# Kernel tuning notes

Measured on AMD Instinct MI355X. Metric: run time of the kernel, lower is better.

Reference implementation:

```python
import jax, jax.numpy as jnp
import numpy as np

D_MODEL = 2048
NUM_HEADS = 16
HEAD_DIM = D_MODEL // NUM_HEADS


def setup_inputs() -> dict:
    key = jax.random.key(0)
    ks = jax.random.split(key, 11)
    B, S = 2, 2048
    s = 1.0 / np.sqrt(D_MODEL)
    return {
        "query": jax.random.normal(ks[0], (B, S, D_MODEL), jnp.float32),
        "key_in": jax.random.normal(ks[1], (B, S, D_MODEL), jnp.float32),
        "value": jax.random.normal(ks[2], (B, S, D_MODEL), jnp.float32),
        "Wq": jax.random.normal(ks[3], (D_MODEL, D_MODEL), jnp.float32) * s,
        "bq": jnp.zeros((D_MODEL,), jnp.float32),
        "Wk": jax.random.normal(ks[4], (D_MODEL, D_MODEL), jnp.float32) * s,
        "bk": jnp.zeros((D_MODEL,), jnp.float32),
        "Wv": jax.random.normal(ks[5], (D_MODEL, D_MODEL), jnp.float32) * s,
        "bv": jnp.zeros((D_MODEL,), jnp.float32),
        "Wo": jax.random.normal(ks[6], (D_MODEL, D_MODEL), jnp.float32) * s,
        "bo": jnp.zeros((D_MODEL,), jnp.float32),
    }


def reference(query, key_in, value, Wq, bq, Wk, bk, Wv, bv, Wo, bo):
    B, S, _ = query.shape
    # projections (torch Linear: x @ W.T + b)
    q = query @ Wq.T + bq
    k = key_in @ Wk.T + bk
    v = value @ Wv.T + bv
    # [B, H, S, Dh]
    q = q.reshape(B, S, NUM_HEADS, HEAD_DIM).transpose(0, 2, 1, 3)
    k = k.reshape(B, -1, NUM_HEADS, HEAD_DIM).transpose(0, 2, 1, 3)
    v = v.reshape(B, -1, NUM_HEADS, HEAD_DIM).transpose(0, 2, 1, 3)
    scores = jnp.einsum("bhqd,bhkd->bhqk", q, k) / np.sqrt(HEAD_DIM).astype(np.float32)
    attn = jax.nn.softmax(scores, axis=-1)
    out = jnp.einsum("bhqk,bhkd->bhqd", attn, v)
    out = out.transpose(0, 2, 1, 3).reshape(B, S, D_MODEL)
    return out @ Wo.T + bo
```

## Files before the change

### kernel.cpp

```cpp
#include <hip/hip_runtime.h>
#include <hip/hip_bf16.h>
#include <stdint.h>

typedef __hip_bfloat16 bf16;
typedef __attribute__((ext_vector_type(8))) short bf16x8;
typedef __attribute__((ext_vector_type(4))) float f32x4;
typedef __attribute__((ext_vector_type(4))) short s16x4;

constexpr int D_MODEL   = 2048;
constexpr int NUM_HEADS = 16;
constexpr int HEAD_DIM  = 128;
constexpr int BATCH     = 2;
constexpr int SEQ       = 2048;

constexpr int GBM = 256, GBN = 128, GBK = 64;
constexpr int G_ABUF = GBM * GBK;
constexpr int G_BBUF = GBN * GBK;
constexpr int G_BUF  = G_ABUF + G_BBUF;
constexpr int G_LDS  = 3 * G_BUF;

__device__ __forceinline__ void gload_lds16(const bf16* g, bf16* l) {
    __builtin_amdgcn_global_load_lds(
        (const __attribute__((address_space(1))) void*)g,
        (__attribute__((address_space(3))) void*)l, 16, 0, 0);
}

typedef __attribute__((address_space(3))) const bf16 lds_cbf16;

struct CvtArgs { const float* src[7]; bf16* dst[7]; int n8[7]; };

__global__ __launch_bounds__(256)
void cvt_multi(CvtArgs a)
{
    const int t = blockIdx.y;
    const float* __restrict__ s = a.src[t];
    bf16* __restrict__ d = a.dst[t];
    const int n8 = a.n8[t];
    for (int i = blockIdx.x * 256 + threadIdx.x; i < n8; i += gridDim.x * 256) {
        f32x4 x = *(const f32x4*)(s + (size_t)i * 8);
        f32x4 y = *(const f32x4*)(s + (size_t)i * 8 + 4);
        bf16 t8[8] = { __float2bfloat16(x[0]), __float2bfloat16(x[1]),
                       __float2bfloat16(x[2]), __float2bfloat16(x[3]),
                       __float2bfloat16(y[0]), __float2bfloat16(y[1]),
                       __float2bfloat16(y[2]), __float2bfloat16(y[3]) };
        *(bf16x8*)(d + (size_t)i * 8) = *(const bf16x8*)t8;
    }
}


#define DS_READ16(A0, B0, A1, B1, vA0, vB0, vA1, vB1)                          \
    asm volatile(                                                              \
        "ds_read_b128 %0, %16 offset:0\n\t"                                    \
        "ds_read_b128 %1, %16 offset:2048\n\t"                                 \
        "ds_read_b128 %2, %16 offset:4096\n\t"                                 \
        "ds_read_b128 %3, %16 offset:6144\n\t"                                 \
        "ds_read_b128 %4, %17 offset:0\n\t"                                    \
        "ds_read_b128 %5, %17 offset:2048\n\t"                                 \
        "ds_read_b128 %6, %17 offset:4096\n\t"                                 \
        "ds_read_b128 %7, %17 offset:6144\n\t"                                 \
        "ds_read_b128 %8, %18 offset:0\n\t"                                    \
        "ds_read_b128 %9, %18 offset:2048\n\t"                                 \
        "ds_read_b128 %10, %18 offset:4096\n\t"                                \
        "ds_read_b128 %11, %18 offset:6144\n\t"                                \
        "ds_read_b128 %12, %19 offset:0\n\t"                                   \
        "ds_read_b128 %13, %19 offset:2048\n\t"                                \
        "ds_read_b128 %14, %19 offset:4096\n\t"                                \
        "ds_read_b128 %15, %19 offset:6144"                                    \
        : "=&v"(A0[0]), "=&v"(A0[1]), "=&v"(A0[2]), "=&v"(A0[3]),              \
          "=&v"(B0[0]), "=&v"(B0[1]), "=&v"(B0[2]), "=&v"(B0[3]),              \
          "=&v"(A1[0]), "=&v"(A1[1]), "=&v"(A1[2]), "=&v"(A1[3]),              \
          "=&v"(B1[0]), "=&v"(B1[1]), "=&v"(B1[2]), "=&v"(B1[3])               \
        : "v"(vA0), "v"(vB0), "v"(vA1), "v"(vB1))

#define MFMA_HALF(AR, BR)                                                      \
    {                                                                          \
        __builtin_amdgcn_s_setprio(1);                                         \
        _Pragma("unroll")                                                      \
        for (int i_ = 0; i_ < 4; i_++)                                         \
            _Pragma("unroll")                                                  \
            for (int j_ = 0; j_ < 4; j_++)                                     \
                acc[i_][j_] = __builtin_amdgcn_mfma_f32_16x16x32_bf16(         \
                    AR[i_], BR[j_], acc[i_][j_], 0, 0, 0);                     \
        __builtin_amdgcn_s_setprio(0);                                         \
        __builtin_amdgcn_sched_barrier(0);                                     \
    }

#define GEMM_TILE(t, CA0, CB0, CA1, CB1, NA0, NB0, NA1, NB1)                   \
    {                                                                          \
        const int  bs_ = (bc + 2 >= 3) ? bc - 1 : bc + 2;                      \
        const bool pf_ = (t) + 2 < NT;                                         \
        if (pf_) { stageA((t) + 2, bs_, 0); stageA((t) + 2, bs_, 1);           \
                   stageA((t) + 2, bs_, 2); stageA((t) + 2, bs_, 3);           \
                   stageB((t) + 2, bs_, 0); stageB((t) + 2, bs_, 1); }         \
        asm volatile("s_waitcnt lgkmcnt(0)" ::: "memory");    \
        __builtin_amdgcn_sched_barrier(0);                                     \
        MFMA_HALF(CA0, CB0);                                                   \
        if (pf_)               asm volatile("s_waitcnt vmcnt(6)" ::: "memory");\
        else if ((t) + 1 < NT) asm volatile("s_waitcnt vmcnt(0)" ::: "memory");\
        asm volatile("s_barrier" ::: "memory");          \
        if ((t) + 1 < NT) {                                                    \
            const int bn_ = (bc + 1 >= 3) ? 0 : bc + 1;                        \
            const uint32_t nA_ = aoffTh + (uint32_t)(bn_ * (G_BUF * 2));       \
            const uint32_t nB_ = boffTh + (uint32_t)(bn_ * (G_BUF * 2));       \
            DS_READ16(NA0, NB0, NA1, NB1, nA_, nB_, nA_ ^ 64u, nB_ ^ 64u);     \
            __builtin_amdgcn_sched_barrier(0);        \
        }                                                                      \
        MFMA_HALF(CA1, CB1);                                                   \
        bc = (bc + 1 == 3) ? 0 : bc + 1;                                       \
    }

template <typename TC, bool TRANS_PERM>
__device__ __forceinline__
void gemm_body(const bf16* __restrict__ A, const bf16* __restrict__ W,
               const float* __restrict__ bias, TC* __restrict__ C,
               int M, int N, int K, bf16* smem)
{
    const int tid  = threadIdx.x;
    const int lane = tid & 63;
    const int wave = tid >> 6;
    const int quad = lane >> 4, l16 = lane & 15;
    const int sw   = l16 & 7;
    const int wr   = wave >> 1;
    const int wc   = wave & 1;
    const int m0   = blockIdx.y * GBM, n0 = blockIdx.x * GBN;

    const int rloc = tid >> 3;
    const int gsw  = (tid & 7) ^ (rloc & 7);
    const int NT   = K / GBK;

    const bf16* Abase = A + (size_t)(m0 + rloc) * K + gsw * 8;
    const bf16* Bbase = W + (size_t)(n0 + rloc) * K + gsw * 8;
    const size_t rstep = (size_t)64 * K;

    auto stageA = [&](int t, int bi, int u) {
        gload_lds16(Abase + u * rstep + (size_t)t * GBK,
                    smem + bi * G_BUF + (u * 512 + tid) * 8);
    };
    auto stageB = [&](int t, int bi, int u) {
        gload_lds16(Bbase + u * rstep + (size_t)t * GBK,
                    smem + bi * G_BUF + G_ABUF + (u * 512 + tid) * 8);
    };

    const uint32_t aoffTh = (uint32_t)(uintptr_t)(lds_cbf16*)
        &smem[(wr * 64 + l16) * 64 + (quad ^ sw) * 8];
    const uint32_t boffTh = (uint32_t)(uintptr_t)(lds_cbf16*)
        &smem[G_ABUF + (wc * 64 + l16) * 64 + (quad ^ sw) * 8];

    f32x4 acc[4][4];
#pragma unroll
    for (int i = 0; i < 4; i++)
#pragma unroll
        for (int j = 0; j < 4; j++) acc[i][j] = (f32x4){0.f, 0.f, 0.f, 0.f};

    bf16x8 pa0[4], pb0[4], pa1[4], pb1[4];
    bf16x8 qa0[4], qb0[4], qa1[4], qb1[4];

#pragma unroll
    for (int u = 0; u < 4; u++) stageA(0, 0, u);
#pragma unroll
    for (int u = 0; u < 2; u++) stageB(0, 0, u);
    if (NT > 1) {
#pragma unroll
        for (int u = 0; u < 4; u++) stageA(1, 1, u);
#pragma unroll
        for (int u = 0; u < 2; u++) stageB(1, 1, u);
        asm volatile("s_waitcnt vmcnt(6)" ::: "memory");
    } else {
        asm volatile("s_waitcnt vmcnt(0)" ::: "memory");
    }
    asm volatile("s_barrier" ::: "memory");
    DS_READ16(pa0, pb0, pa1, pb1, aoffTh, boffTh, aoffTh ^ 64u, boffTh ^ 64u);
    __builtin_amdgcn_sched_barrier(0);

    int bc = 0;
    for (int t = 0; t < NT; t += 2) {
        GEMM_TILE(t,     pa0, pb0, pa1, pb1,  qa0, qb0, qa1, qb1);
        GEMM_TILE(t + 1, qa0, qb0, qa1, qb1,  pa0, pb0, pa1, pb1);
    }

#pragma unroll
    for (int j = 0; j < 4; j++) {
        const int col = n0 + wc * 64 + j * 16 + l16;
        const float bv = bias[col];
#pragma unroll
        for (int i = 0; i < 4; i++) {
            const int row0 = m0 + wr * 64 + i * 16 + quad * 4;
            if constexpr (TRANS_PERM) {
                int g   = row0 & 63;
                int tau = g >> 4, qh = (g >> 2) & 3;
                int pp  = (tau >> 1) * 32 + qh * 8 + (tau & 1) * 4;
                int sp  = ((row0 & 2047) & ~63) | pp;
                size_t idx = (size_t)(row0 >> 11) * ((size_t)D_MODEL * SEQ)
                           + (size_t)col * SEQ + sp;
                bf16 t4[4];
#pragma unroll
                for (int r = 0; r < 4; r++) t4[r] = __float2bfloat16(acc[i][j][r] + bv);
                *(s16x4*)&C[idx] = *(const s16x4*)t4;
            } else {
#pragma unroll
                for (int r = 0; r < 4; r++) {
                    int row = row0 + r;
                    if constexpr (sizeof(TC) == 2)
                        C[(size_t)row * N + col] = (TC)__float2bfloat16(acc[i][j][r] + bv);
                    else
                        C[(size_t)row * N + col] = (TC)(acc[i][j][r] + bv);
                }
            }
        }
    }
}

template <typename TC, bool TRANS_PERM>
__global__ __launch_bounds__(512, 2)
void gemm_bf16(const bf16* __restrict__ A, const bf16* __restrict__ W,
               const float* __restrict__ bias, TC* __restrict__ C,
               int M, int N, int K)
{
    __shared__ bf16 smem[G_LDS];
    gemm_body<TC, TRANS_PERM>(A, W, bias, C, M, N, K, smem);
}

struct QkvArgs { const bf16* A[3]; const bf16* W[3]; const float* bias[3]; bf16* C[3]; };

__global__ __launch_bounds__(512, 2)
void gemm_qkv(QkvArgs ga, int M, int N, int K)
{
    __shared__ bf16 smem[G_LDS];
    const int z = blockIdx.z;
    if (z == 2) gemm_body<bf16, true >(ga.A[2], ga.W[2], ga.bias[2], ga.C[2], M, N, K, smem);
    else        gemm_body<bf16, false>(ga.A[z], ga.W[z], ga.bias[z], ga.C[z], M, N, K, smem);
}

struct QkArgs { const bf16* A[2]; const bf16* W[2]; const float* bias[2]; bf16* C[2]; };

__global__ __launch_bounds__(512, 2)
void gemm_qk(QkArgs ga, int M, int N, int K)
{
    __shared__ bf16 smem[G_LDS];
    const int z = blockIdx.z;
    gemm_body<bf16, false>(ga.A[z], ga.W[z], ga.bias[z], ga.C[z], M, N, K, smem);
}

__global__ __launch_bounds__(256)
void flash_attn_kernel(const bf16* __restrict__ Qp, const bf16* __restrict__ Kp,
                       const bf16* __restrict__ Vt, bf16* __restrict__ Op)
{
    constexpr int BQ = 128, BKV = 64, DH = 128;
    __shared__ bf16 sK[2][BKV * DH];
    __shared__ bf16 sV[2][DH * BKV];

    const int tid  = threadIdx.x;
    const int wave = tid >> 6, lane = tid & 63;
    const int quad = lane >> 4, l16 = lane & 15;
    const int q0 = blockIdx.x * BQ;
    const int h  = blockIdx.y;
    const int b  = blockIdx.z;

    const size_t base  = (size_t)b * SEQ * D_MODEL + (size_t)h * HEAD_DIM;
    const size_t basev = ((size_t)b * NUM_HEADS + h) * (size_t)HEAD_DIM * SEQ;
    const bf16* Kb = Kp + base;
    const bf16* Vb = Vt + basev;

    auto stage = [&](int t, int bi) {
        const bf16* Kt = Kb + (size_t)t * BKV * D_MODEL;
        const bf16* Vtile = Vb + (size_t)t * BKV;
        bf16* sKb = sK[bi];
        bf16* sVb = sV[bi];
#pragma unroll
        for (int s = 0; s < 4; s++) {
            int c = s * 256 + wave * 64 + lane;
            int row = c >> 4, gs = c & 15;
            int g = gs ^ (row & 15);
            gload_lds16(Kt + (size_t)row * D_MODEL + g * 8, sKb + (size_t)c * 8);
        }
#pragma unroll
        for (int s = 0; s < 4; s++) {
            int c = s * 256 + wave * 64 + lane;
            int dh = c >> 3, gs = c & 7;
            int g = gs ^ (dh & 7);
            gload_lds16(Vtile + (size_t)dh * SEQ + g * 8, sVb + (size_t)c * 8);
        }
    };

    bf16x8 bq[2][4];
#pragma unroll
    for (int nt = 0; nt < 2; nt++)
#pragma unroll
        for (int kk = 0; kk < 4; kk++)
            bq[nt][kk] = *(const bf16x8*)&Qp[base +
                (size_t)(q0 + wave * 32 + nt * 16 + l16) * D_MODEL + kk * 32 + quad * 8];

    f32x4 oacc[2][8];
#pragma unroll
    for (int nt = 0; nt < 2; nt++)
#pragma unroll
        for (int mt = 0; mt < 8; mt++) oacc[nt][mt] = (f32x4){0.f, 0.f, 0.f, 0.f};

    float lsum[2] = {0.f, 0.f};

    const float SCL2E = 0.08838834764831845f * 1.4426950408889634f;
    constexpr int NT = SEQ / BKV;

    stage(0, 0);

    for (int t = 0; t < NT; ++t) {
        __syncthreads();
        if (t + 1 < NT) stage(t + 1, (t + 1) & 1);

        const bf16* sKc = sK[t & 1];
        const bf16* sVc = sV[t & 1];

        f32x4 sacc[2][4];
#pragma unroll
        for (int nt = 0; nt < 2; nt++)
#pragma unroll
            for (int kt = 0; kt < 4; kt++) sacc[nt][kt] = (f32x4){0.f, 0.f, 0.f, 0.f};
#pragma unroll
        for (int kk = 0; kk < 4; kk++) {
            bf16x8 ak[4];
#pragma unroll
            for (int kt = 0; kt < 4; kt++) {
                int row = kt * 16 + l16;
                int g   = (kk * 4 + quad) ^ l16;
                ak[kt] = *(const bf16x8*)&sKc[(size_t)row * DH + g * 8];
            }
#pragma unroll
            for (int nt = 0; nt < 2; nt++)
#pragma unroll
                for (int kt = 0; kt < 4; kt++)
                    sacc[nt][kt] = __builtin_amdgcn_mfma_f32_16x16x32_bf16(ak[kt], bq[nt][kk], sacc[nt][kt], 0, 0, 0);
        }

        bf16x8 pb[2][2];
#pragma unroll
        for (int nt = 0; nt < 2; nt++) {
            bf16 tmp[16];
#pragma unroll
            for (int kt = 0; kt < 4; kt++) {
#pragma unroll
                for (int r = 0; r < 4; r++) {
                    float p = exp2f(fminf(sacc[nt][kt][r] * SCL2E, 60.f));
                    lsum[nt] += p;
                    tmp[(kt >> 1) * 8 + (kt & 1) * 4 + r] = __float2bfloat16(p);
                }
            }
            pb[nt][0] = *(const bf16x8*)&tmp[0];
            pb[nt][1] = *(const bf16x8*)&tmp[8];
        }

#pragma unroll
        for (int c = 0; c < 2; c++) {
#pragma unroll
            for (int mt = 0; mt < 8; mt++) {
                int row = mt * 16 + l16;
                int g   = (c * 4 + quad) ^ (l16 & 7);
                bf16x8 av = *(const bf16x8*)&sVc[(size_t)row * BKV + g * 8];
#pragma unroll
                for (int nt = 0; nt < 2; nt++)
                    oacc[nt][mt] = __builtin_amdgcn_mfma_f32_16x16x32_bf16(av, pb[nt][c], oacc[nt][mt], 0, 0, 0);
            }
        }
    }

#pragma unroll
    for (int nt = 0; nt < 2; nt++) {
        float v = lsum[nt];
        v += __shfl_xor(v, 16);
        v += __shfl_xor(v, 32);
        lsum[nt] = v;
    }

#pragma unroll
    for (int nt = 0; nt < 2; nt++) {
        float inv = 1.f / lsum[nt];
        int row = q0 + wave * 32 + nt * 16 + l16;
#pragma unroll
        for (int mt = 0; mt < 8; mt++) {
            bf16 t4[4];
#pragma unroll
            for (int r = 0; r < 4; r++) t4[r] = __float2bfloat16(oacc[nt][mt][r] * inv);
            *(s16x4*)&Op[base + (size_t)row * D_MODEL + mt * 16 + quad * 4] = *(const s16x4*)t4;
        }
    }
}

extern "C" void kernel_launch(void* const* d_in, const int* in_sizes, int n_in,
                              void* d_out, int out_size, void* d_ws, size_t ws_size,
                              hipStream_t stream)
{
    const float* query  = (const float*)d_in[0];
    const float* key_in = (const float*)d_in[1];
    const float* value  = (const float*)d_in[2];
    const float* Wq = (const float*)d_in[3];
    const float* bq = (const float*)d_in[4];
    const float* Wk = (const float*)d_in[5];
    const float* bk = (const float*)d_in[6];
    const float* Wv = (const float*)d_in[7];
    const float* bv = (const float*)d_in[8];
    const float* Wo = (const float*)d_in[9];
    const float* bo = (const float*)d_in[10];
    float* out = (float*)d_out;

    const int tokens = BATCH * SEQ;
    const size_t nAct = (size_t)tokens * D_MODEL;
    const size_t nW   = (size_t)D_MODEL * D_MODEL;

    const bool fused_qkv = ws_size >= (6 * nAct + 4 * nW) * sizeof(bf16);

    bf16* p = (bf16*)d_ws;
    bf16* qb  = p; p += nAct;
    bf16* kb  = p; p += nAct;
    bf16* vb  = p; p += nAct;
    bf16* wqb = p; p += nW;
    bf16* wkb = p; p += nW;
    bf16* wvb = p; p += nW;
    bf16* wob = p; p += nW;
    bf16* qp  = p; p += nAct;
    bf16* kp  = p; p += nAct;
    bf16* vpT;
    if (fused_qkv) { vpT = p; p += nAct; }
    else           { vpT = qb; }
    bf16* ap = fused_qkv ? qb : kb;

    CvtArgs ca;
    ca.src[0] = query;  ca.dst[0] = qb;  ca.n8[0] = (int)(nAct / 8);
    ca.src[1] = key_in; ca.dst[1] = kb;  ca.n8[1] = (int)(nAct / 8);
    ca.src[2] = value;  ca.dst[2] = vb;  ca.n8[2] = (int)(nAct / 8);
    ca.src[3] = Wq;     ca.dst[3] = wqb; ca.n8[3] = (int)(nW / 8);
    ca.src[4] = Wk;     ca.dst[4] = wkb; ca.n8[4] = (int)(nW / 8);
    ca.src[5] = Wv;     ca.dst[5] = wvb; ca.n8[5] = (int)(nW / 8);
    ca.src[6] = Wo;     ca.dst[6] = wob; ca.n8[6] = (int)(nW / 8);
    cvt_multi<<<dim3(512, 7), 256, 0, stream>>>(ca);

    if (fused_qkv) {
        QkvArgs qa;
        qa.A[0] = qb; qa.W[0] = wqb; qa.bias[0] = bq; qa.C[0] = qp;
        qa.A[1] = kb; qa.W[1] = wkb; qa.bias[1] = bk; qa.C[1] = kp;
        qa.A[2] = vb; qa.W[2] = wvb; qa.bias[2] = bv; qa.C[2] = vpT;
        dim3 g3(D_MODEL / 128, tokens / 256, 3);
        gemm_qkv<<<g3, 512, 0, stream>>>(qa, tokens, D_MODEL, D_MODEL);
    } else {
        QkArgs qa;
        qa.A[0] = qb; qa.W[0] = wqb; qa.bias[0] = bq; qa.C[0] = qp;
        qa.A[1] = kb; qa.W[1] = wkb; qa.bias[1] = bk; qa.C[1] = kp;
        dim3 g2(D_MODEL / 128, tokens / 256, 2);
        gemm_qk<<<g2, 512, 0, stream>>>(qa, tokens, D_MODEL, D_MODEL);
        dim3 gg(D_MODEL / 128, tokens / 256);
        gemm_bf16<bf16, true><<<gg, 512, 0, stream>>>(vb, wvb, bv, vpT, tokens, D_MODEL, D_MODEL);
    }

    dim3 ga(SEQ / 128, NUM_HEADS, BATCH);
    flash_attn_kernel<<<ga, 256, 0, stream>>>(qp, kp, vpT, ap);

    dim3 gg(D_MODEL / 128, tokens / 256);
    gemm_bf16<float, false><<<gg, 512, 0, stream>>>(ap, wob, bo, out, tokens, D_MODEL, D_MODEL);
}
```

Measured before the change: 445.8 us.

## Software-pipeline flash attention: overlap QK of next tile with softmax·V of previous

Restructures the attention main loop so the QK^T MFMAs for tile t are issued alongside the exp/softmax and PV MFMAs for tile t-1. Two score buffers alternate, and the loop is unrolled by two. K and V staging are split so K is prefetched one tile further ahead than V. s_setprio raises wave priority around the MFMA blocks to help interleaving across waves. The goal is to hide exp/VALU and LDS latency behind matrix work, at the cost of extra registers for the second score buffer and a more complex prologue and epilogue.

```diff
diff --git a/kernel.cpp b/kernel.cpp
--- a/kernel.cpp
+++ b/kernel.cpp
@@ -241,6 +241,67 @@
     gemm_body<bf16, false>(ga.A[z], ga.W[z], ga.bias[z], ga.C[z], M, N, K, smem);
 }
 
+
+#define QK_TILE(tt, SC)                                                        \
+    {                                                                          \
+        _Pragma("unroll")                                                      \
+        for (int nt_ = 0; nt_ < 2; nt_++)                                      \
+            _Pragma("unroll")                                                  \
+            for (int kt_ = 0; kt_ < 4; kt_++)                                  \
+                SC[nt_][kt_] = (f32x4){0.f, 0.f, 0.f, 0.f};                    \
+        const bf16* sKc_ = sK[(tt) & 1];                                       \
+        __builtin_amdgcn_s_setprio(1);                                         \
+        _Pragma("unroll")                                                      \
+        for (int kk_ = 0; kk_ < 4; kk_++) {                                    \
+            bf16x8 ak_[4];                                                     \
+            _Pragma("unroll")                                                  \
+            for (int kt_ = 0; kt_ < 4; kt_++) {                                \
+                int row_ = kt_ * 16 + l16;                                     \
+                int g_   = (kk_ * 4 + quad) ^ l16;                             \
+                ak_[kt_] = *(const bf16x8*)&sKc_[(size_t)row_ * DH + g_ * 8];  \
+            }                                                                  \
+            _Pragma("unroll")                                                  \
+            for (int nt_ = 0; nt_ < 2; nt_++)                                  \
+                _Pragma("unroll")                                              \
+                for (int kt_ = 0; kt_ < 4; kt_++)                              \
+                    SC[nt_][kt_] = __builtin_amdgcn_mfma_f32_16x16x32_bf16(    \
+                        ak_[kt_], bq[nt_][kk_], SC[nt_][kt_], 0, 0, 0);        \
+        }                                                                      \
+        __builtin_amdgcn_s_setprio(0);                                         \
+        __builtin_amdgcn_sched_barrier(0);       \
+    }
+
+#define SMPV_TILE(tt, SP)                                                      \
+    {                                                                          \
+        bf16x8 pb_[2][2];                                                      \
+        _Pragma("unroll")                                                      \
+        for (int nt_ = 0; nt_ < 2; nt_++)                                      \
+            _Pragma("unroll")                                                  \
+            for (int kt_ = 0; kt_ < 4; kt_++)                                  \
+                _Pragma("unroll")                                              \
+                for (int r_ = 0; r_ < 4; r_++) {                               \
+                    float p_ = exp2f(fminf(SP[nt_][kt_][r_] * SCL2E, 60.f));   \
+                    lsum[nt_] += p_;                                           \
+                    pb_[nt_][kt_ >> 1][(kt_ & 1) * 4 + r_] =                   \
+                        __builtin_bit_cast(short, __float2bfloat16(p_));       \
+                }                                                              \
+        const bf16* sVc_ = sV[(tt) & 1];                                       \
+        __builtin_amdgcn_s_setprio(1);                                         \
+        _Pragma("unroll")                                                      \
+        for (int c_ = 0; c_ < 2; c_++)                                         \
+            _Pragma("unroll")                                                  \
+            for (int mt_ = 0; mt_ < 8; mt_++) {                                \
+                int row_ = mt_ * 16 + l16;                                     \
+                int g_   = (c_ * 4 + quad) ^ (l16 & 7);                        \
+                bf16x8 av_ = *(const bf16x8*)&sVc_[(size_t)row_ * BKV + g_ * 8];\
+                _Pragma("unroll")                                              \
+                for (int nt_ = 0; nt_ < 2; nt_++)                              \
+                    oacc[nt_][mt_] = __builtin_amdgcn_mfma_f32_16x16x32_bf16(  \
+                        av_, pb_[nt_][c_], oacc[nt_][mt_], 0, 0, 0);           \
+            }                                                                  \
+        __builtin_amdgcn_s_setprio(0);                                         \
+    }
+
 __global__ __launch_bounds__(256)
 void flash_attn_kernel(const bf16* __restrict__ Qp, const bf16* __restrict__ Kp,
                        const bf16* __restrict__ Vt, bf16* __restrict__ Op)
@@ -261,11 +322,9 @@
     const bf16* Kb = Kp + base;
     const bf16* Vb = Vt + basev;
 
-    auto stage = [&](int t, int bi) {
+    auto stageK = [&](int t) {
         const bf16* Kt = Kb + (size_t)t * BKV * D_MODEL;
-        const bf16* Vtile = Vb + (size_t)t * BKV;
-        bf16* sKb = sK[bi];
-        bf16* sVb = sV[bi];
+        bf16* sKb = sK[t & 1];
 #pragma unroll
         for (int s = 0; s < 4; s++) {
             int c = s * 256 + wave * 64 + lane;
@@ -273,6 +332,10 @@
             int g = gs ^ (row & 15);
             gload_lds16(Kt + (size_t)row * D_MODEL + g * 8, sKb + (size_t)c * 8);
         }
+    };
+    auto stageV = [&](int t) {
+        const bf16* Vtile = Vb + (size_t)t * BKV;
+        bf16* sVb = sV[t & 1];
 #pragma unroll
         for (int s = 0; s < 4; s++) {
             int c = s * 256 + wave * 64 + lane;
@@ -301,66 +364,33 @@
     const float SCL2E = 0.08838834764831845f * 1.4426950408889634f;
     constexpr int NT = SEQ / BKV;
 
-    stage(0, 0);
-
-    for (int t = 0; t < NT; ++t) {
+    f32x4 saccP[2][4], saccQ[2][4];
+
+    stageK(0);
+    __syncthreads();
+    stageK(1);
+    stageV(0);
+    QK_TILE(0, saccP)
+
+    for (int t = 1; t + 1 < NT; t += 2) {
         __syncthreads();
-        if (t + 1 < NT) stage(t + 1, (t + 1) & 1);
-
-        const bf16* sKc = sK[t & 1];
-        const bf16* sVc = sV[t & 1];
-
-        f32x4 sacc[2][4];
-#pragma unroll
-        for (int nt = 0; nt < 2; nt++)
-#pragma unroll
-            for (int kt = 0; kt < 4; kt++) sacc[nt][kt] = (f32x4){0.f, 0.f, 0.f, 0.f};
-#pragma unroll
-        for (int kk = 0; kk < 4; kk++) {
-            bf16x8 ak[4];
-#pragma unroll
-            for (int kt = 0; kt < 4; kt++) {
-                int row = kt * 16 + l16;
-                int g   = (kk * 4 + quad) ^ l16;
-                ak[kt] = *(const bf16x8*)&sKc[(size_t)row * DH + g * 8];
-            }
-#pragma unroll
-            for (int nt = 0; nt < 2; nt++)
-#pragma unroll
-                for (int kt = 0; kt < 4; kt++)
-                    sacc[nt][kt] = __builtin_amdgcn_mfma_f32_16x16x32_bf16(ak[kt], bq[nt][kk], sacc[nt][kt], 0, 0, 0);
-        }
-
-        bf16x8 pb[2][2];
-#pragma unroll
-        for (int nt = 0; nt < 2; nt++) {
-            bf16 tmp[16];
-#pragma unroll
-            for (int kt = 0; kt < 4; kt++) {
-#pragma unroll
-                for (int r = 0; r < 4; r++) {
-                    float p = exp2f(fminf(sacc[nt][kt][r] * SCL2E, 60.f));
-                    lsum[nt] += p;
-                    tmp[(kt >> 1) * 8 + (kt & 1) * 4 + r] = __float2bfloat16(p);
-                }
-            }
-            pb[nt][0] = *(const bf16x8*)&tmp[0];
-            pb[nt][1] = *(const bf16x8*)&tmp[8];
-        }
-
-#pragma unroll
-        for (int c = 0; c < 2; c++) {
-#pragma unroll
-            for (int mt = 0; mt < 8; mt++) {
-                int row = mt * 16 + l16;
-                int g   = (c * 4 + quad) ^ (l16 & 7);
-                bf16x8 av = *(const bf16x8*)&sVc[(size_t)row * BKV + g * 8];
-#pragma unroll
-                for (int nt = 0; nt < 2; nt++)
-                    oacc[nt][mt] = __builtin_amdgcn_mfma_f32_16x16x32_bf16(av, pb[nt][c], oacc[nt][mt], 0, 0, 0);
-            }
-        }
-    }
+        stageK(t + 1);
+        stageV(t);
+        QK_TILE(t, saccQ)
+        SMPV_TILE(t - 1, saccP)
+
+        __syncthreads();
+        if (t + 2 < NT) stageK(t + 2);
+        stageV(t + 1);
+        QK_TILE(t + 1, saccP)
+        SMPV_TILE(t, saccQ)
+    }
+    __syncthreads();
+    stageV(NT - 1);
+    QK_TILE(NT - 1, saccQ)
+    SMPV_TILE(NT - 2, saccP)
+    __syncthreads();
+    SMPV_TILE(NT - 1, saccQ)
 
 #pragma unroll
     for (int nt = 0; nt < 2; nt++) {
```

Measured after the change: 476.3 us. 6.8% more time.
